# Kernel tuning notes

Hardware: AMD Instinct MI355X
Metric: run time of the kernel (lower is better)

## Reference

```python
import jax, jax.numpy as jnp
import numpy as np

EPS = 1e-5

def inorm(x):
    # instance norm over time (last) axis; torch.std is unbiased (ddof=1)
    m = jnp.mean(x, axis=-1, keepdims=True)
    s = jnp.sqrt(jnp.var(x, axis=-1, ddof=1, keepdims=True))
    return (x - m) / (s + EPS)

def tinorm(x):
    # time-wise instance norm: normalize over channel axis (dim=1)
    m = jnp.mean(x, axis=1, keepdims=True)
    s = jnp.sqrt(jnp.var(x, axis=1, ddof=1, keepdims=True))
    return (x - m) / (s + EPS)

def adaptive_norm(src, trg, wq, wk, wv, norm_fn):
    # src, trg: [B,C,T]; wq/wk/wv: [out,in] as in nn.Linear
    temp = src.shape[1] ** 0.5
    q = jnp.einsum('bct,oc->bto', norm_fn(src), wq)        # [B,Ts,C]
    k = jnp.einsum('bct,oc->bto', norm_fn(trg), wk)        # [B,Tt,C]
    v = jnp.einsum('bct,oc->bto', trg, wv)                 # [B,Tt,C]
    attn = jax.nn.softmax(jnp.einsum('bsc,btc->bst', q / temp, k), axis=-1)
    mean = jnp.einsum('bst,btc->bsc', attn, v)             # attn-weighted mean
    var = jax.nn.relu(jnp.einsum('bst,btc->bsc', attn, v * v) - mean * mean)
    mean_c = jnp.mean(mean, axis=1)[:, :, None]            # [B,C,1]
    std_c = jnp.sqrt(jnp.mean(var, axis=1))[:, :, None]    # [B,C,1]
    return std_c * inorm(src) + mean_c

def sap(x, w, b):
    # self-attention pooling over axis 1; x: [B,N,C], w: [C], b: [1]
    a = jax.nn.softmax(jnp.einsum('bnc,c->bn', x, w) + b, axis=-1)
    return jnp.einsum('bnc,bn->bc', x, a)

def setup_inputs():
    key = jax.random.key(0)
    ks = jax.random.split(key, 24)
    B, C, Ts, Tt, S = 4, 512, 2048, 2048, 2048
    sc = 1.0 / np.sqrt(C).astype(np.float32)
    return {
        'src': jax.random.normal(ks[0], (B, C, Ts), jnp.float32),
        'trg': jax.random.normal(ks[1], (B, C, Tt), jnp.float32),
        'means': jax.random.normal(ks[2], (B, S, C), jnp.float32),
        'stds': jax.random.uniform(ks[3], (B, S, C), jnp.float32),
        'wq_t': jax.random.normal(ks[4], (C, C), jnp.float32) * sc,
        'wk_t': jax.random.normal(ks[5], (C, C), jnp.float32) * sc,
        'wv_t': jax.random.normal(ks[6], (C, C), jnp.float32) * sc,
        'wq_c': jax.random.normal(ks[7], (C, C), jnp.float32) * sc,
        'wk_c': jax.random.normal(ks[8], (C, C), jnp.float32) * sc,
        'wv_c': jax.random.normal(ks[9], (C, C), jnp.float32) * sc,
        'conv1_w': jax.random.normal(ks[10], (C, 2 * C), jnp.float32) * sc,
        'conv1_b': jax.random.normal(ks[11], (C,), jnp.float32) * 0.02,
        'conv2_w': jax.random.normal(ks[12], (C, C, 3), jnp.float32) * sc,
        'bn_g': jax.random.uniform(ks[13], (C,), jnp.float32, 0.5, 1.5),
        'bn_b': jax.random.normal(ks[14], (C,), jnp.float32) * 0.05,
        'bn_m': jax.random.normal(ks[15], (C,), jnp.float32) * 0.1,
        'bn_v': jax.random.uniform(ks[16], (C,), jnp.float32, 0.5, 1.5),
        'msap_w': jax.random.normal(ks[17], (C,), jnp.float32) * sc,
        'msap_b': jax.random.normal(ks[18], (1,), jnp.float32) * 0.02,
        'ssap_w': jax.random.normal(ks[19], (C,), jnp.float32) * sc,
        'ssap_b': jax.random.normal(ks[20], (1,), jnp.float32) * 0.02,
    }

def reference(src, trg, means, stds, wq_t, wk_t, wv_t, wq_c, wk_c, wv_c,
              conv1_w, conv1_b, conv2_w, bn_g, bn_b, bn_m, bn_v,
              msap_w, msap_b, ssap_w, ssap_b):
    src1 = adaptive_norm(src, trg, wq_t, wk_t, wv_t, tinorm)   # TAN
    src2 = adaptive_norm(src, trg, wq_c, wk_c, wv_c, inorm)    # CAN
    x = jnp.concatenate([src1, src2], axis=1)                  # [B,2C,T]
    # conv1: kernel_size=1 -> pointwise GEMM
    x = jnp.einsum('bct,oc->bot', x, conv1_w) + conv1_b[None, :, None]
    # conv2: Conv1d(k=3, pad=1, bias=False) + BatchNorm1d(eval) + ReLU
    x = jax.lax.conv_general_dilated(x, conv2_w, (1,), 'SAME',
                                     dimension_numbers=('NCH', 'OIH', 'NCH'))
    x = (x - bn_m[None, :, None]) * jax.lax.rsqrt(bn_v[None, :, None] + EPS)
    x = x * bn_g[None, :, None] + bn_b[None, :, None]
    x = jax.nn.relu(x)
    # GLAN
    mean = sap(means, msap_w, msap_b)[:, :, None]              # [B,C,1]
    std = sap(stds, ssap_w, ssap_b)[:, :, None]                # [B,C,1]
    return inorm(x) * std + mean
```

## Files before the change

kernel.cpp:

```cpp
#include <hip/hip_runtime.h>
#include <cstdint>
#include <cstddef>

#define B_ 4
#define C_ 512
#define T_ 2048
#define S_ 2048
#define EPSF 1e-5f

typedef __bf16 bf16;
typedef __attribute__((ext_vector_type(8))) __bf16 bf16x8;
typedef __attribute__((ext_vector_type(4))) float f32x4;

__device__ __forceinline__ bf16 f2b(float f){ return (bf16)f; }
__device__ __forceinline__ float b2f(bf16 h){ return (float)h; }

__device__ __forceinline__ void gl_lds16(const void* g, void* l){
  __builtin_amdgcn_global_load_lds((__attribute__((address_space(1))) void*)(g),
                                   (__attribute__((address_space(3))) void*)(l), 16, 0, 0);
}

__device__ __forceinline__ float wave_sum(float v){
#pragma unroll
  for (int o = 32; o; o >>= 1) v += __shfl_xor(v, o, 64);
  return v;
}
__device__ __forceinline__ float wave_max(float v){
#pragma unroll
  for (int o = 32; o; o >>= 1) v = fmaxf(v, __shfl_xor(v, o, 64));
  return v;
}

template<int EPI, int TNW>
__global__ void __launch_bounds__(256) gemm_nt(
    const bf16* __restrict__ A, const bf16* __restrict__ Bm, void* __restrict__ Cout,
    int K, int lda, int ldb, int ldc,
    long long sA, long long sB, long long sC, long long sCb,
    int zdivA, int zmodB, float scale,
    const float* __restrict__ rs, const float* __restrict__ rsh,
    const float* __restrict__ cbias,
    float* __restrict__ osum, float* __restrict__ osum2)
{
  constexpr int TN = TNW*32;
  __shared__ alignas(16) bf16 lA[128*64];
  __shared__ alignas(16) bf16 lB[TN*64];
  const int tid = threadIdx.x;
  const int z = blockIdx.z;
  const bf16* Ab = A + (long long)(z / zdivA) * sA;
  const bf16* Bb = Bm + (long long)(z % zmodB) * sB;
  const int m0 = blockIdx.y*128, n0 = blockIdx.x*TN;
  const int lane = tid & 63, wvi = tid >> 6;
  const int wm = wvi >> 1, wn = wvi & 1;

  f32x4 acc[4][TNW] = {};

  const int lrow = tid >> 3;
  const int lcol = ((tid ^ lrow) & 7) * 8;
  const bf16* pa = Ab + (long long)(m0 + lrow)*lda + lcol;
  const bf16* pb = Bb + (long long)(n0 + lrow)*ldb + lcol;
  char* sa = (char*)lA + tid*16;
  char* sb = (char*)lB + tid*16;

  for (int k0 = 0; k0 < K; k0 += 64) {
#pragma unroll
    for (int it = 0; it < 4; ++it)
      gl_lds16(pa + (long long)it*32*lda + k0, sa + it*4096);
#pragma unroll
    for (int it = 0; it < TNW; ++it)
      gl_lds16(pb + (long long)it*32*ldb + k0, sb + it*4096);
    __syncthreads();
#pragma unroll
    for (int ks = 0; ks < 2; ++ks) {
      const int kq = ks*4 + (lane >> 4);
      bf16x8 af[4], bfr[TNW];
#pragma unroll
      for (int mt = 0; mt < 4; ++mt) {
        int r = wm*64 + mt*16 + (lane & 15);
        af[mt] = *(const bf16x8*)&lA[r*64 + ((kq ^ (r & 7))*8)];
      }
#pragma unroll
      for (int nt = 0; nt < TNW; ++nt) {
        int r = wn*(TNW*16) + nt*16 + (lane & 15);
        bfr[nt] = *(const bf16x8*)&lB[r*64 + ((kq ^ (r & 7))*8)];
      }
#pragma unroll
      for (int mt = 0; mt < 4; ++mt)
#pragma unroll
        for (int nt = 0; nt < TNW; ++nt)
          acc[mt][nt] = __builtin_amdgcn_mfma_f32_16x16x32_bf16(af[mt], bfr[nt], acc[mt][nt], 0, 0, 0);
    }
    __syncthreads();
  }

  if (EPI == 3) {
    __shared__ float red1[4][TNW][16], red2[4][TNW][16];
    float s1[TNW], s2[TNW];
#pragma unroll
    for (int nt = 0; nt < TNW; ++nt) {
      s1[nt] = 0.f; s2[nt] = 0.f;
#pragma unroll
      for (int mt = 0; mt < 4; ++mt)
#pragma unroll
        for (int i = 0; i < 4; ++i) {
          float v = acc[mt][nt][i];
          s1[nt] += v; s2[nt] += v*v;
        }
      s1[nt] += __shfl_xor(s1[nt], 16, 64);
      s1[nt] += __shfl_xor(s1[nt], 32, 64);
      s2[nt] += __shfl_xor(s2[nt], 16, 64);
      s2[nt] += __shfl_xor(s2[nt], 32, 64);
    }
    if (lane < 16) {
#pragma unroll
      for (int nt = 0; nt < TNW; ++nt) {
        red1[wvi][nt][lane] = s1[nt];
        red2[wvi][nt][lane] = s2[nt];
      }
    }
    __syncthreads();
    if (tid < 2*TN) {
      const int which = tid >= TN;
      const int col = tid - which*TN;
      const int wn2 = col / (TNW*16), rem = col % (TNW*16);
      const float* rr = which ? &red2[0][0][0] : &red1[0][0][0];
      float v = rr[wn2*(TNW*16) + rem] + rr[(2+wn2)*(TNW*16) + rem];
      float* dst = which ? osum2 : osum;
      atomicAdd(&dst[sCb*z + n0 + col], v);
    }
    return;
  }

  const int cr = (lane >> 4)*4, cc = lane & 15;
#pragma unroll
  for (int mt = 0; mt < 4; ++mt) {
#pragma unroll
    for (int i = 0; i < 4; ++i) {
      const int mm = m0 + wm*64 + mt*16 + cr + i;
#pragma unroll
      for (int nt = 0; nt < TNW; ++nt) {
        const int nn = n0 + wn*(TNW*16) + nt*16 + cc;
        float v = acc[mt][nt][i];
        const long long co = sC*z + (long long)mm*ldc + nn;
        if (EPI == 0) {
          v *= scale;
          if (cbias) v += cbias[sCb*z + nn];
          ((bf16*)Cout)[co] = f2b(v);
        } else if (EPI == 1) {
          ((float*)Cout)[co] = v;
        } else {
          ((float*)Cout)[co] = fmaxf(v*rs[mm] + rsh[mm], 0.f);
        }
      }
    }
  }
}

__global__ void __launch_bounds__(256) row_stats_k(const float* __restrict__ X1,
    const float* __restrict__ X2, float* __restrict__ Mo, float* __restrict__ So, int n1)
{
  __shared__ float r1[4], r2[4];
  const int row = blockIdx.x;
  const float* x = (row < n1) ? X1 + (long long)row*T_ : X2 + (long long)(row-n1)*T_;
  float s1 = 0.f, s2 = 0.f;
  for (int i = threadIdx.x; i < T_; i += 256){ float v = x[i]; s1 += v; s2 += v*v; }
  s1 = wave_sum(s1); s2 = wave_sum(s2);
  const int lane = threadIdx.x & 63, w = threadIdx.x >> 6;
  if (!lane){ r1[w] = s1; r2[w] = s2; }
  __syncthreads();
  if (threadIdx.x == 0){
    s1 = r1[0]+r1[1]+r1[2]+r1[3];
    s2 = r2[0]+r2[1]+r2[2]+r2[3];
    float m = s1 * (1.f/T_);
    float var = (s2 - s1*m) * (1.f/(T_-1));
    Mo[row] = m; So[row] = sqrtf(fmaxf(var, 0.f));
  }
}

__global__ void __launch_bounds__(256) col_stats_k(const float* __restrict__ src,
    const float* __restrict__ trg, float* __restrict__ Mo, float* __restrict__ So)
{
  __shared__ float r1[4][64], r2[4][64];
  const int z = blockIdx.y, t0 = blockIdx.x*64;
  const float* X = (z < B_) ? src : trg;
  const int b = z & (B_-1);
  const int tl = threadIdx.x & 63, cg = threadIdx.x >> 6;
  float s1 = 0.f, s2 = 0.f;
  for (int c = cg; c < C_; c += 4) {
    float v = X[((long long)b*C_ + c)*T_ + t0 + tl];
    s1 += v; s2 += v*v;
  }
  r1[cg][tl] = s1; r2[cg][tl] = s2;
  __syncthreads();
  if (cg == 0) {
    s1 = r1[0][tl]+r1[1][tl]+r1[2][tl]+r1[3][tl];
    s2 = r2[0][tl]+r2[1][tl]+r2[2][tl]+r2[3][tl];
    float m = s1 * (1.f/C_);
    float var = (s2 - s1*m) * (1.f/(C_-1));
    Mo[z*T_ + t0 + tl] = m;
    So[z*T_ + t0 + tl] = sqrtf(fmaxf(var, 0.f));
  }
}

__global__ void __launch_bounds__(256) transform_k(const float* __restrict__ src,
    const float* __restrict__ trg,
    const float* __restrict__ tnm, const float* __restrict__ tns,
    const float* __restrict__ inm, const float* __restrict__ ins,
    bf16* __restrict__ NSt, bf16* __restrict__ NSc,
    bf16* __restrict__ NTt, bf16* __restrict__ NTc, bf16* __restrict__ TTr)
{
  __shared__ float tile[32][33];
  const int z = blockIdx.z, t0 = blockIdx.x*32, c0 = blockIdx.y*32;
  const int is_t = z >= B_, b = z & (B_-1);
  const float* X = is_t ? trg : src;
  const int tx = threadIdx.x, ty = threadIdx.y;
#pragma unroll
  for (int r = 0; r < 4; ++r) {
    int ci = ty + r*8;
    tile[ci][tx] = X[((long long)b*C_ + c0 + ci)*T_ + t0 + tx];
  }
  __syncthreads();
#pragma unroll
  for (int r = 0; r < 4; ++r) {
    int tj = ty + r*8, ci = tx;
    float v = tile[ci][tj];
    int gt = t0 + tj, gc = c0 + ci;
    float a = (v - tnm[z*T_ + gt]) / (tns[z*T_ + gt] + EPSF);
    float d = (v - inm[z*C_ + gc]) / (ins[z*C_ + gc] + EPSF);
    long long o = ((long long)b*T_ + gt)*C_ + gc;
    if (is_t) { NTt[o] = f2b(a); NTc[o] = f2b(d); TTr[o] = f2b(v); }
    else      { NSt[o] = f2b(a); NSc[o] = f2b(d); }
  }
}

__global__ void __launch_bounds__(256) softmax_inplace_k(bf16* __restrict__ P)
{
  __shared__ float red[4];
  const long long row = blockIdx.x;
  bf16* x = P + row*T_ + threadIdx.x*8;
  bf16x8 a = *(const bf16x8*)x;
  float v[8];
#pragma unroll
  for (int j = 0; j < 8; ++j) v[j] = b2f(a[j]);
  float m = -3.4e38f;
#pragma unroll
  for (int j = 0; j < 8; ++j) m = fmaxf(m, v[j]);
  m = wave_max(m);
  const int lane = threadIdx.x & 63, w = threadIdx.x >> 6;
  if (!lane) red[w] = m;
  __syncthreads();
  m = fmaxf(fmaxf(red[0], red[1]), fmaxf(red[2], red[3]));
  __syncthreads();
  float s = 0.f;
#pragma unroll
  for (int j = 0; j < 8; ++j){ v[j] = __expf(v[j] - m); s += v[j]; }
  s = wave_sum(s);
  if (!lane) red[w] = s;
  __syncthreads();
  s = red[0]+red[1]+red[2]+red[3];
  const float inv = 1.f/s;
#pragma unroll
  for (int j = 0; j < 8; ++j) a[j] = f2b(v[j]*inv);
  *(bf16x8*)x = a;
}

__global__ void __launch_bounds__(256) softmax_row_k(const float* __restrict__ X, float* __restrict__ O)
{
  __shared__ float red[4];
  const long long row = blockIdx.x;
  const float* x = X + row*T_ + threadIdx.x*8;
  float v[8];
  f32x4 a0 = *(const f32x4*)x;
  f32x4 a1 = *(const f32x4*)(x + 4);
#pragma unroll
  for (int j = 0; j < 4; ++j){ v[j] = a0[j]; v[4+j] = a1[j]; }
  float m = -3.4e38f;
#pragma unroll
  for (int j = 0; j < 8; ++j) m = fmaxf(m, v[j]);
  m = wave_max(m);
  const int lane = threadIdx.x & 63, w = threadIdx.x >> 6;
  if (!lane) red[w] = m;
  __syncthreads();
  m = fmaxf(fmaxf(red[0], red[1]), fmaxf(red[2], red[3]));
  __syncthreads();
  float s = 0.f;
#pragma unroll
  for (int j = 0; j < 8; ++j){ v[j] = __expf(v[j] - m); s += v[j]; }
  s = wave_sum(s);
  if (!lane) red[w] = s;
  __syncthreads();
  s = red[0]+red[1]+red[2]+red[3];
  const float inv = 1.f/s;
  float* o = O + row*T_ + threadIdx.x*8;
#pragma unroll
  for (int j = 0; j < 8; ++j) o[j] = v[j]*inv;
}

__global__ void __launch_bounds__(256) colsum_k(const bf16* __restrict__ P, float* __restrict__ cs)
{
  const int t = blockIdx.x*256 + threadIdx.x;
  const int z = blockIdx.z;
  const long long s0 = (long long)blockIdx.y*256;
  const bf16* p = P + ((long long)z*S_ + s0)*T_ + t;
  float a = 0.f;
  for (int s = 0; s < 256; ++s) a += b2f(p[(long long)s*T_]);
  atomicAdd(&cs[z*T_ + t], a);
}

__global__ void __launch_bounds__(256) vv_fin_k(const float* __restrict__ cs,
    const bf16* __restrict__ VT, const float* __restrict__ msum,
    const float* __restrict__ m2sum, float* __restrict__ meanc, float* __restrict__ stdc)
{
  __shared__ float r1[4];
  const int c = blockIdx.x, z = blockIdx.y;
  const bf16* vr = VT + ((long long)z*C_ + c)*T_;
  const float* w = cs + z*T_;
  float a = 0.f;
  for (int t = threadIdx.x; t < T_; t += 256){ float v = b2f(vr[t]); a += w[t]*v*v; }
  a = wave_sum(a);
  const int lane = threadIdx.x & 63, wq = threadIdx.x >> 6;
  if (!lane) r1[wq] = a;
  __syncthreads();
  if (threadIdx.x == 0){
    a = r1[0]+r1[1]+r1[2]+r1[3];
    const int idx = z*C_ + c;
    meanc[idx] = msum[idx] * (1.f/S_);
    float var = (a - m2sum[idx]) * (1.f/S_);
    stdc[idx] = sqrtf(fmaxf(var, 0.f));
  }
}

__global__ void __launch_bounds__(256) weff_k(const float* __restrict__ w1,
    const float* __restrict__ b1, const float* __restrict__ sdt, const float* __restrict__ sdc,
    const float* __restrict__ mct, const float* __restrict__ mcc,
    bf16* __restrict__ Weff, float* __restrict__ beff)
{
  __shared__ float r1[4];
  const int o = blockIdx.x, b = blockIdx.y;
  float accb = 0.f;
  for (int c = threadIdx.x; c < C_; c += 256) {
    float wa = w1[o*2*C_ + c], wb = w1[o*2*C_ + C_ + c];
    Weff[((long long)(b*C_ + o))*C_ + c] = f2b(wa*sdt[b*C_+c] + wb*sdc[b*C_+c]);
    accb += wa*mct[b*C_+c] + wb*mcc[b*C_+c];
  }
  accb = wave_sum(accb);
  const int lane = threadIdx.x & 63, w = threadIdx.x >> 6;
  if (!lane) r1[w] = accb;
  __syncthreads();
  if (threadIdx.x == 0) beff[b*C_ + o] = b1[o] + r1[0]+r1[1]+r1[2]+r1[3];
}

__global__ void __launch_bounds__(256) w2r_k(const float* __restrict__ w2,
    const float* __restrict__ g, const float* __restrict__ be,
    const float* __restrict__ mu, const float* __restrict__ va,
    bf16* __restrict__ W2r, float* __restrict__ bnsc, float* __restrict__ bnsh)
{
  const int o = blockIdx.x;
  for (int c = threadIdx.x; c < C_; c += 256)
#pragma unroll
    for (int dt = 0; dt < 3; ++dt)
      W2r[(long long)o*3*C_ + dt*C_ + c] = f2b(w2[((long long)o*C_ + c)*3 + dt]);
  if (threadIdx.x == 0) {
    float s = g[o] * rsqrtf(va[o] + EPSF);
    bnsc[o] = s;
    bnsh[o] = be[o] - mu[o]*s;
  }
}

__global__ void __launch_bounds__(256) cast6_k(const float* __restrict__ a0,
    const float* __restrict__ a1, const float* __restrict__ a2, const float* __restrict__ a3,
    const float* __restrict__ a4, const float* __restrict__ a5, bf16* __restrict__ o)
{
  const int i = blockIdx.x*256 + threadIdx.x;
  const int slot = i >> 18;
  const float* srcs[6] = {a0,a1,a2,a3,a4,a5};
  const float sc = (slot < 2) ? 0.044194173824159216f : 1.f;
  o[i] = f2b(srcs[slot][i & 262143] * sc);
}

__global__ void __launch_bounds__(256) zero_pad_k(bf16* __restrict__ x1p)
{
  const int i = blockIdx.x*256 + threadIdx.x;
  const int b = i >> 10, rem = i & 1023;
  const long long row = (rem >> 9) ? (T_+1) : 0;
  const int c = rem & (C_-1);
  x1p[((long long)b*(T_+2) + row)*C_ + c] = f2b(0.f);
}

__global__ void __launch_bounds__(256) zero_f32_k(float* __restrict__ p)
{
  p[blockIdx.x*256 + threadIdx.x] = 0.f;
}

__global__ void __launch_bounds__(256) sap_logit_k(const float* __restrict__ means,
    const float* __restrict__ stds, const float* __restrict__ mw, const float* __restrict__ sw,
    const float* __restrict__ mb, const float* __restrict__ sb, float* __restrict__ out)
{
  const int n = blockIdx.x*4 + (threadIdx.x >> 6);
  const int z = blockIdx.y;
  const int sel = z >= B_, b = z & (B_-1);
  const float* x = sel ? stds : means;
  const float* w = sel ? sw : mw;
  const int lane = threadIdx.x & 63;
  const float* p = x + ((long long)b*S_ + n)*C_;
  float a = 0.f;
  for (int c = lane; c < C_; c += 64) a += p[c]*w[c];
  a = wave_sum(a);
  if (!lane) out[z*S_ + n] = a + (sel ? sb[0] : mb[0]);
}

__global__ void __launch_bounds__(256) sap_wsum_k(const float* __restrict__ means,
    const float* __restrict__ stds, const float* __restrict__ a, float* __restrict__ out)
{
  const int c = blockIdx.x*256 + threadIdx.x;
  const int z = blockIdx.z;
  const int sel = z >= B_, b = z & (B_-1);
  const float* x = sel ? stds : means;
  const long long n0 = (long long)blockIdx.y*256;
  const float* p = x + ((long long)b*S_ + n0)*C_ + c;
  const float* aw = a + z*S_ + n0;
  float acc = 0.f;
  for (int n = 0; n < 256; ++n) acc += p[(long long)n*C_] * aw[n];
  atomicAdd(&out[z*C_ + c], acc);
}

__global__ void __launch_bounds__(256) final_k(const float* __restrict__ y,
    const float* __restrict__ ym, const float* __restrict__ ys,
    const float* __restrict__ sapms, float* __restrict__ out)
{
  const long long i = (long long)(blockIdx.x*256 + threadIdx.x) * 4;
  const long long r = i >> 11;
  const float m = ym[r], inv = 1.f/(ys[r] + EPSF);
  const float mn = sapms[r], sd = sapms[B_*C_ + r];
  const f32x4 v = *(const f32x4*)(y + i);
  f32x4 o;
#pragma unroll
  for (int j = 0; j < 4; ++j) o[j] = (v[j] - m)*inv*sd + mn;
  *(f32x4*)(out + i) = o;
}

extern "C" void kernel_launch(void* const* d_in, const int* in_sizes, int n_in,
                              void* d_out, int out_size, void* d_ws, size_t ws_size,
                              hipStream_t stream)
{
  (void)in_sizes; (void)n_in; (void)out_size; (void)ws_size;
  const float* src    = (const float*)d_in[0];
  const float* trg    = (const float*)d_in[1];
  const float* means  = (const float*)d_in[2];
  const float* stds   = (const float*)d_in[3];
  const float* conv1w = (const float*)d_in[10];
  const float* conv1b = (const float*)d_in[11];
  const float* conv2w = (const float*)d_in[12];
  const float* bn_g   = (const float*)d_in[13];
  const float* bn_b   = (const float*)d_in[14];
  const float* bn_m   = (const float*)d_in[15];
  const float* bn_v   = (const float*)d_in[16];
  const float* msap_w = (const float*)d_in[17];
  const float* msap_b = (const float*)d_in[18];
  const float* ssap_w = (const float*)d_in[19];
  const float* ssap_b = (const float*)d_in[20];

  const long long BTC = (long long)B_*T_*C_;

  char* p = (char*)d_ws;
  auto take = [&](size_t n)->char*{ char* r = p; p += (n + 255) & ~(size_t)255; return r; };

  bf16* NSc = (bf16*)take(BTC*2);
  bf16* P2  = (bf16*)take((size_t)2*B_*S_*T_*2);
  bf16* NSt = P2;
  bf16* NTc = P2 + BTC;
  bf16* NTt = P2 + 2*BTC;
  bf16* TTr = P2 + 3*BTC;
  bf16* QK4 = (bf16*)take((size_t)4*BTC*2);
  bf16* VT2 = (bf16*)take((size_t)2*BTC*2);
  bf16* WQb = (bf16*)take((size_t)6*C_*C_*2);
  bf16* Weff= (bf16*)take((size_t)B_*C_*C_*2);
  bf16* W2r = (bf16*)take((size_t)C_*3*C_*2);
  bf16* x1p = (bf16*)take((size_t)B_*(T_+2)*C_*2);
  float* y  = (float*)take((size_t)B_*C_*T_*4);
  float* colsum = (float*)take(2*B_*T_*4);
  float* msum   = (float*)take(2*B_*C_*4);
  float* m2sum  = (float*)take(2*B_*C_*4);
  float* sapms  = (float*)take(2*B_*C_*4);
  float* tnm = (float*)take(2*B_*T_*4);
  float* tns = (float*)take(2*B_*T_*4);
  float* inm = (float*)take(2*B_*C_*4);
  float* ins = (float*)take(2*B_*C_*4);
  float* meanc = (float*)take(2*B_*C_*4);
  float* stdc  = (float*)take(2*B_*C_*4);
  float* beff  = (float*)take(B_*C_*4);
  float* bnsc  = (float*)take(C_*4);
  float* bnsh  = (float*)take(C_*4);
  float* ym    = (float*)take(B_*C_*4);
  float* ys    = (float*)take(B_*C_*4);
  float* sapl  = (float*)take(2*B_*S_*4);
  float* sapa  = (float*)take(2*B_*S_*4);

  dim3 blk(256);

  cast6_k<<<6144, blk, 0, stream>>>((const float*)d_in[7], (const float*)d_in[4],
      (const float*)d_in[8], (const float*)d_in[5], (const float*)d_in[9],
      (const float*)d_in[6], WQb);
  w2r_k<<<C_, blk, 0, stream>>>(conv2w, bn_g, bn_b, bn_m, bn_v, W2r, bnsc, bnsh);
  row_stats_k<<<2*B_*C_, blk, 0, stream>>>(src, trg, inm, ins, B_*C_);
  col_stats_k<<<dim3(T_/64, 2*B_), blk, 0, stream>>>(src, trg, tnm, tns);
  transform_k<<<dim3(T_/32, C_/32, 2*B_), dim3(32,8), 0, stream>>>(src, trg,
      tnm, tns, inm, ins, NSt, NSc, NTt, NTc, TTr);
  zero_pad_k<<<16, blk, 0, stream>>>(x1p);
  zero_f32_k<<<112, blk, 0, stream>>>(colsum);

  gemm_nt<0,4><<<dim3(C_/128, (B_*T_)/128, 4), blk, 0, stream>>>(NSc, WQb, QK4,
      C_, C_, C_, C_, BTC, (long long)C_*C_, BTC, 0, 1, 8, 1.f,
      nullptr, nullptr, nullptr, nullptr, nullptr);
  gemm_nt<0,2><<<dim3(T_/64, C_/128, 8), blk, 0, stream>>>(WQb + (size_t)4*C_*C_, TTr, VT2,
      C_, C_, C_, T_, (long long)C_*C_, (long long)T_*C_, (long long)C_*T_, 0, 4, 4, 1.f,
      nullptr, nullptr, nullptr, nullptr, nullptr);
  gemm_nt<0,4><<<dim3(T_/128, T_/128, 8), blk, 0, stream>>>(QK4, QK4 + 2*BTC, P2,
      C_, C_, C_, T_, (long long)T_*C_, (long long)T_*C_, (long long)S_*T_, 0, 1, 8, 1.f,
      nullptr, nullptr, nullptr, nullptr, nullptr);
  softmax_inplace_k<<<2*B_*S_, blk, 0, stream>>>(P2);
  colsum_k<<<dim3(T_/256, S_/256, 8), blk, 0, stream>>>(P2, colsum);
  gemm_nt<3,4><<<dim3(C_/128, S_/128, 8), blk, 0, stream>>>(P2, VT2, nullptr,
      T_, T_, T_, 0, (long long)S_*T_, (long long)C_*T_, 0, C_, 1, 8, 1.f,
      nullptr, nullptr, nullptr, msum, m2sum);
  vv_fin_k<<<dim3(C_, 2*B_), blk, 0, stream>>>(colsum, VT2, msum, m2sum, meanc, stdc);

  weff_k<<<dim3(C_, B_), blk, 0, stream>>>(conv1w, conv1b,
      stdc + B_*C_, stdc, meanc + B_*C_, meanc, Weff, beff);
  gemm_nt<0,2><<<dim3(C_/64, T_/128, B_), blk, 0, stream>>>(NSc, Weff, x1p + C_,
      C_, C_, C_, C_, (long long)T_*C_, (long long)C_*C_, (long long)(T_+2)*C_, C_,
      1, 8, 1.f, nullptr, nullptr, beff, nullptr, nullptr);
  gemm_nt<2,2><<<dim3(T_/64, C_/128, B_), blk, 0, stream>>>(W2r, x1p, y,
      3*C_, 3*C_, C_, T_, 0, (long long)(T_+2)*C_, (long long)C_*T_, 0,
      1, 8, 1.f, bnsc, bnsh, nullptr, nullptr, nullptr);
  row_stats_k<<<B_*C_, blk, 0, stream>>>(y, nullptr, ym, ys, B_*C_);

  sap_logit_k<<<dim3(S_/4, 2*B_), blk, 0, stream>>>(means, stds, msap_w, ssap_w,
      msap_b, ssap_b, sapl);
  softmax_row_k<<<2*B_, blk, 0, stream>>>(sapl, sapa);
  sap_wsum_k<<<dim3(C_/256, S_/256, 2*B_), blk, 0, stream>>>(means, stds, sapa, sapms);

  final_k<<<4096, blk, 0, stream>>>(y, ym, ys, sapms, (float*)d_out);
}
```

Before: 463.9 us.

## Fuse softmax exp into QK GEMM epilogue and y row stats into conv GEMM

```diff
diff --git a/kernel.cpp b/kernel.cpp
--- a/kernel.cpp
+++ b/kernel.cpp
@@ -39,7 +39,7 @@
     int zdivA, int zmodB, float scale,
     const float* __restrict__ rs, const float* __restrict__ rsh,
     const float* __restrict__ cbias,
-    float* __restrict__ osum, float* __restrict__ osum2)
+    float* __restrict__ osum, float* __restrict__ osum2, long long sRs)
 {
   constexpr int TN = TNW*32;
   __shared__ alignas(16) bf16 lA[128*64];
@@ -93,7 +93,15 @@
   }
 
   if (EPI == 3) {
-    __shared__ float red1[4][TNW][16], red2[4][TNW][16];
+    float* red1 = (float*)lA;
+    float* red2 = red1 + 4*TNW*16;
+    const int cr = (lane >> 4)*4;
+    float linv[4][4];
+#pragma unroll
+    for (int mt = 0; mt < 4; ++mt)
+#pragma unroll
+      for (int i = 0; i < 4; ++i)
+        linv[mt][i] = 1.f / rs[(long long)z*sRs + (m0 + wm*64 + mt*16 + cr + i)];
     float s1[TNW], s2[TNW];
 #pragma unroll
     for (int nt = 0; nt < TNW; ++nt) {
@@ -102,7 +110,7 @@
       for (int mt = 0; mt < 4; ++mt)
 #pragma unroll
         for (int i = 0; i < 4; ++i) {
-          float v = acc[mt][nt][i];
+          float v = acc[mt][nt][i] * linv[mt][i];
           s1[nt] += v; s2[nt] += v*v;
         }
       s1[nt] += __shfl_xor(s1[nt], 16, 64);
@@ -113,8 +121,8 @@
     if (lane < 16) {
 #pragma unroll
       for (int nt = 0; nt < TNW; ++nt) {
-        red1[wvi][nt][lane] = s1[nt];
-        red2[wvi][nt][lane] = s2[nt];
+        red1[(wvi*TNW + nt)*16 + lane] = s1[nt];
+        red2[(wvi*TNW + nt)*16 + lane] = s2[nt];
       }
     }
     __syncthreads();
@@ -122,7 +130,7 @@
       const int which = tid >= TN;
       const int col = tid - which*TN;
       const int wn2 = col / (TNW*16), rem = col % (TNW*16);
-      const float* rr = which ? &red2[0][0][0] : &red1[0][0][0];
+      const float* rr = which ? red2 : red1;
       float v = rr[wn2*(TNW*16) + rem] + rr[(2+wn2)*(TNW*16) + rem];
       float* dst = which ? osum2 : osum;
       atomicAdd(&dst[sCb*z + n0 + col], v);
@@ -136,6 +144,7 @@
 #pragma unroll
     for (int i = 0; i < 4; ++i) {
       const int mm = m0 + wm*64 + mt*16 + cr + i;
+      float rsum = 0.f, rsum2 = 0.f;
 #pragma unroll
       for (int nt = 0; nt < TNW; ++nt) {
         const int nn = n0 + wn*(TNW*16) + nt*16 + cc;
@@ -145,10 +154,26 @@
           v *= scale;
           if (cbias) v += cbias[sCb*z + nn];
           ((bf16*)Cout)[co] = f2b(v);
-        } else if (EPI == 1) {
+        } else if (EPI == 2) {
+          v = fmaxf(v*rs[mm] + rsh[mm], 0.f);
           ((float*)Cout)[co] = v;
-        } else {
-          ((float*)Cout)[co] = fmaxf(v*rs[mm] + rsh[mm], 0.f);
+          rsum += v; rsum2 += v*v;
+        } else if (EPI == 4) {
+          v = __expf(v);
+          ((bf16*)Cout)[co] = f2b(v);
+          rsum += v;
+        }
+      }
+      if (EPI == 2 || EPI == 4) {
+        rsum += __shfl_xor(rsum, 1, 64); rsum += __shfl_xor(rsum, 2, 64);
+        rsum += __shfl_xor(rsum, 4, 64); rsum += __shfl_xor(rsum, 8, 64);
+        if (EPI == 2) {
+          rsum2 += __shfl_xor(rsum2, 1, 64); rsum2 += __shfl_xor(rsum2, 2, 64);
+          rsum2 += __shfl_xor(rsum2, 4, 64); rsum2 += __shfl_xor(rsum2, 8, 64);
+        }
+        if (cc == 0) {
+          atomicAdd(&osum[(long long)z*sRs + mm], rsum);
+          if (EPI == 2) atomicAdd(&osum2[(long long)z*sRs + mm], rsum2);
         }
       }
     }
@@ -232,37 +257,6 @@
   }
 }
 
-__global__ void __launch_bounds__(256) softmax_inplace_k(bf16* __restrict__ P)
-{
-  __shared__ float red[4];
-  const long long row = blockIdx.x;
-  bf16* x = P + row*T_ + threadIdx.x*8;
-  bf16x8 a = *(const bf16x8*)x;
-  float v[8];
-#pragma unroll
-  for (int j = 0; j < 8; ++j) v[j] = b2f(a[j]);
-  float m = -3.4e38f;
-#pragma unroll
-  for (int j = 0; j < 8; ++j) m = fmaxf(m, v[j]);
-  m = wave_max(m);
-  const int lane = threadIdx.x & 63, w = threadIdx.x >> 6;
-  if (!lane) red[w] = m;
-  __syncthreads();
-  m = fmaxf(fmaxf(red[0], red[1]), fmaxf(red[2], red[3]));
-  __syncthreads();
-  float s = 0.f;
-#pragma unroll
-  for (int j = 0; j < 8; ++j){ v[j] = __expf(v[j] - m); s += v[j]; }
-  s = wave_sum(s);
-  if (!lane) red[w] = s;
-  __syncthreads();
-  s = red[0]+red[1]+red[2]+red[3];
-  const float inv = 1.f/s;
-#pragma unroll
-  for (int j = 0; j < 8; ++j) a[j] = f2b(v[j]*inv);
-  *(bf16x8*)x = a;
-}
-
 __global__ void __launch_bounds__(256) softmax_row_k(const float* __restrict__ X, float* __restrict__ O)
 {
   __shared__ float red[4];
@@ -295,14 +289,18 @@
   for (int j = 0; j < 8; ++j) o[j] = v[j]*inv;
 }
 
-__global__ void __launch_bounds__(256) colsum_k(const bf16* __restrict__ P, float* __restrict__ cs)
-{
+__global__ void __launch_bounds__(256) colsum_k(const bf16* __restrict__ P,
+    const float* __restrict__ l, float* __restrict__ cs)
+{
+  __shared__ float linv[256];
   const int t = blockIdx.x*256 + threadIdx.x;
   const int z = blockIdx.z;
   const long long s0 = (long long)blockIdx.y*256;
+  linv[threadIdx.x] = 1.f / l[(long long)z*S_ + s0 + threadIdx.x];
+  __syncthreads();
   const bf16* p = P + ((long long)z*S_ + s0)*T_ + t;
   float a = 0.f;
-  for (int s = 0; s < 256; ++s) a += b2f(p[(long long)s*T_]);
+  for (int s = 0; s < 256; ++s) a += b2f(p[(long long)s*T_]) * linv[s];
   atomicAdd(&cs[z*T_ + t], a);
 }
 
@@ -424,12 +422,15 @@
 }
 
 __global__ void __launch_bounds__(256) final_k(const float* __restrict__ y,
-    const float* __restrict__ ym, const float* __restrict__ ys,
+    const float* __restrict__ ysum, const float* __restrict__ y2sum,
     const float* __restrict__ sapms, float* __restrict__ out)
 {
   const long long i = (long long)(blockIdx.x*256 + threadIdx.x) * 4;
   const long long r = i >> 11;
-  const float m = ym[r], inv = 1.f/(ys[r] + EPSF);
+  const float s1 = ysum[r], s2 = y2sum[r];
+  const float m = s1 * (1.f/T_);
+  const float var = (s2 - s1*m) * (1.f/(T_-1));
+  const float inv = 1.f/(sqrtf(fmaxf(var, 0.f)) + EPSF);
   const float mn = sapms[r], sd = sapms[B_*C_ + r];
   const f32x4 v = *(const f32x4*)(y + i);
   f32x4 o;
@@ -481,6 +482,9 @@
   float* msum   = (float*)take(2*B_*C_*4);
   float* m2sum  = (float*)take(2*B_*C_*4);
   float* sapms  = (float*)take(2*B_*C_*4);
+  float* lrow   = (float*)take(2*B_*S_*4);
+  float* ysum   = (float*)take(B_*C_*4);
+  float* y2sum  = (float*)take(B_*C_*4);
   float* tnm = (float*)take(2*B_*T_*4);
   float* tns = (float*)take(2*B_*T_*4);
   float* inm = (float*)take(2*B_*C_*4);
@@ -490,8 +494,6 @@
   float* beff  = (float*)take(B_*C_*4);
   float* bnsc  = (float*)take(C_*4);
   float* bnsh  = (float*)take(C_*4);
-  float* ym    = (float*)take(B_*C_*4);
-  float* ys    = (float*)take(B_*C_*4);
   float* sapl  = (float*)take(2*B_*S_*4);
   float* sapa  = (float*)take(2*B_*S_*4);
 
@@ -506,38 +508,36 @@
   transform_k<<<dim3(T_/32, C_/32, 2*B_), dim3(32,8), 0, stream>>>(src, trg,
       tnm, tns, inm, ins, NSt, NSc, NTt, NTc, TTr);
   zero_pad_k<<<16, blk, 0, stream>>>(x1p);
-  zero_f32_k<<<112, blk, 0, stream>>>(colsum);
+  zero_f32_k<<<192, blk, 0, stream>>>(colsum);
 
   gemm_nt<0,4><<<dim3(C_/128, (B_*T_)/128, 4), blk, 0, stream>>>(NSc, WQb, QK4,
       C_, C_, C_, C_, BTC, (long long)C_*C_, BTC, 0, 1, 8, 1.f,
-      nullptr, nullptr, nullptr, nullptr, nullptr);
+      nullptr, nullptr, nullptr, nullptr, nullptr, 0);
   gemm_nt<0,2><<<dim3(T_/64, C_/128, 8), blk, 0, stream>>>(WQb + (size_t)4*C_*C_, TTr, VT2,
       C_, C_, C_, T_, (long long)C_*C_, (long long)T_*C_, (long long)C_*T_, 0, 4, 4, 1.f,
-      nullptr, nullptr, nullptr, nullptr, nullptr);
-  gemm_nt<0,4><<<dim3(T_/128, T_/128, 8), blk, 0, stream>>>(QK4, QK4 + 2*BTC, P2,
+      nullptr, nullptr, nullptr, nullptr, nullptr, 0);
+  gemm_nt<4,4><<<dim3(T_/128, T_/128, 8), blk, 0, stream>>>(QK4, QK4 + 2*BTC, P2,
       C_, C_, C_, T_, (long long)T_*C_, (long long)T_*C_, (long long)S_*T_, 0, 1, 8, 1.f,
-      nullptr, nullptr, nullptr, nullptr, nullptr);
-  softmax_inplace_k<<<2*B_*S_, blk, 0, stream>>>(P2);
-  colsum_k<<<dim3(T_/256, S_/256, 8), blk, 0, stream>>>(P2, colsum);
+      nullptr, nullptr, nullptr, lrow, nullptr, S_);
+  colsum_k<<<dim3(T_/256, S_/256, 8), blk, 0, stream>>>(P2, lrow, colsum);
   gemm_nt<3,4><<<dim3(C_/128, S_/128, 8), blk, 0, stream>>>(P2, VT2, nullptr,
       T_, T_, T_, 0, (long long)S_*T_, (long long)C_*T_, 0, C_, 1, 8, 1.f,
-      nullptr, nullptr, nullptr, msum, m2sum);
+      lrow, nullptr, nullptr, msum, m2sum, S_);
   vv_fin_k<<<dim3(C_, 2*B_), blk, 0, stream>>>(colsum, VT2, msum, m2sum, meanc, stdc);
 
   weff_k<<<dim3(C_, B_), blk, 0, stream>>>(conv1w, conv1b,
       stdc + B_*C_, stdc, meanc + B_*C_, meanc, Weff, beff);
   gemm_nt<0,2><<<dim3(C_/64, T_/128, B_), blk, 0, stream>>>(NSc, Weff, x1p + C_,
       C_, C_, C_, C_, (long long)T_*C_, (long long)C_*C_, (long long)(T_+2)*C_, C_,
-      1, 8, 1.f, nullptr, nullptr, beff, nullptr, nullptr);
+      1, 8, 1.f, nullptr, nullptr, beff, nullptr, nullptr, 0);
   gemm_nt<2,2><<<dim3(T_/64, C_/128, B_), blk, 0, stream>>>(W2r, x1p, y,
       3*C_, 3*C_, C_, T_, 0, (long long)(T_+2)*C_, (long long)C_*T_, 0,
-      1, 8, 1.f, bnsc, bnsh, nullptr, nullptr, nullptr);
-  row_stats_k<<<B_*C_, blk, 0, stream>>>(y, nullptr, ym, ys, B_*C_);
+      1, 8, 1.f, bnsc, bnsh, nullptr, ysum, y2sum, C_);
 
   sap_logit_k<<<dim3(S_/4, 2*B_), blk, 0, stream>>>(means, stds, msap_w, ssap_w,
       msap_b, ssap_b, sapl);
   softmax_row_k<<<2*B_, blk, 0, stream>>>(sapl, sapa);
   sap_wsum_k<<<dim3(C_/256, S_/256, 2*B_), blk, 0, stream>>>(means, stds, sapa, sapms);
 
-  final_k<<<4096, blk, 0, stream>>>(y, ym, ys, sapms, (float*)d_out);
-}
+  final_k<<<4096, blk, 0, stream>>>(y, ysum, y2sum, sapms, (float*)d_out);
+}
```

New measurement: 453.4 us. -2.3%, faster.
